# Optimization experiments

Hardware: AMD Instinct MI355X
Metric: run time of the kernel (lower is better)

The kernel has to match this reference:

```python
import jax, jax.numpy as jnp
import numpy as np

B_SZ, N_IN, N_CTX, UNITS, RANK = 4096, 4096, 512, 4096, 256


def setup_inputs() -> dict:
    key = jax.random.key(0)
    ks = jax.random.split(key, 8)
    inputs = jax.random.normal(ks[0], (B_SZ, N_IN), dtype=jnp.float32)
    context = jax.random.normal(ks[1], (B_SZ, N_CTX), dtype=jnp.float32)
    # Orthogonal-ish init approximated by scaled normals (math-equivalent shapes)
    U = jax.random.normal(ks[2], (N_IN, RANK), dtype=jnp.float32) / np.sqrt(N_IN)
    S = jax.random.uniform(ks[3], (RANK,), dtype=jnp.float32, minval=0.5, maxval=1.5)
    V = jax.random.normal(ks[4], (UNITS, RANK), dtype=jnp.float32) / np.sqrt(UNITS)
    W = jax.random.normal(ks[5], (N_CTX, RANK), dtype=jnp.float32) / np.sqrt(N_CTX)
    B = jnp.zeros((RANK,), dtype=jnp.float32)
    bias = jnp.zeros((UNITS,), dtype=jnp.float32)
    return {"inputs": inputs, "context": context, "U": U, "S": S, "V": V, "W": W, "B": B, "bias": bias}


def reference(inputs, context, U, S, V, W, B, bias):
    # chi[b,r] = sigmoid(context @ W + B)
    chi = jax.nn.sigmoid(context @ W + B)                  # [B, R]
    # Original: kernel[b,n,m] = sum_r U[n,r]*S[r]*chi[b,r]*V[m,r];
    # out[b,m] = sum_n x[b,n]*kernel[b,n,m]. Algebraically equal to:
    t = (inputs @ U) * (S * chi)                           # [B, R]
    out = t @ V.T + bias                                   # first '+ self.bias'
    out = out + bias                                       # 'outputs += self.bias' (use_bias=True)
    return jax.nn.relu(out)
```

## Files before the change

kernel.cpp:

```cpp
#include <hip/hip_runtime.h>

#define B_SZ 4096
#define N_IN 4096
#define N_CTX 512
#define UNITS 4096
#define RANK 256
#define ZSPLIT 8

typedef __attribute__((ext_vector_type(8))) __bf16 bf16x8;
typedef __attribute__((ext_vector_type(4))) float f32x4;
typedef __attribute__((ext_vector_type(8))) unsigned short ushort8;

__device__ __forceinline__ unsigned short f2bf(float f) {
    unsigned int u = __float_as_uint(f);
    u += 0x7FFFu + ((u >> 16) & 1u);
    return (unsigned short)(u >> 16);
}
__device__ __forceinline__ unsigned short f2bf_fast(float f) {
    return (unsigned short)((__float_as_uint(f) + 0x8000u) >> 16);
}
__device__ __forceinline__ float bf2f(unsigned short h) {
    return __uint_as_float(((unsigned int)h) << 16);
}
__device__ __forceinline__ bf16x8 ldfrag(const unsigned short* p) {
    ushort8 t = *(const ushort8*)p;
    return __builtin_bit_cast(bf16x8, t);
}
__device__ __forceinline__ bf16x8 cvt8(float4 lo, float4 hi) {
    ushort8 t = { f2bf_fast(lo.x), f2bf_fast(lo.y), f2bf_fast(lo.z), f2bf_fast(lo.w),
                  f2bf_fast(hi.x), f2bf_fast(hi.y), f2bf_fast(hi.z), f2bf_fast(hi.w) };
    return __builtin_bit_cast(bf16x8, t);
}
#define MFMA(a, b, c) __builtin_amdgcn_mfma_f32_16x16x32_bf16((a), (b), (c), 0, 0, 0)

__global__ void prep(const float* __restrict__ U, const float* __restrict__ W,
                     const float* __restrict__ V,
                     unsigned short* __restrict__ UT, unsigned short* __restrict__ WT,
                     unsigned short* __restrict__ Vb) {
    __shared__ unsigned short t[64][66];
    int bid = blockIdx.x, tid = threadIdx.x;
    if (bid < 288) {
        const float* src; unsigned short* dst; int R, C, rb, cb;
        if (bid < 256) { src = U; dst = UT; R = N_IN; C = RANK; rb = (bid & 63) * 64; cb = (bid >> 6) * 64; }
        else { int b = bid - 256; src = W; dst = WT; R = N_CTX; C = RANK; rb = (b & 7) * 64; cb = (b >> 3) * 64; }
        int r = tid >> 4, c4 = (tid & 15) * 4;
        for (int i = 0; i < 4; i++) {
            float4 v = *(const float4*)(src + (size_t)(rb + r + i * 16) * C + cb + c4);
            t[r + i * 16][c4 + 0] = f2bf(v.x);
            t[r + i * 16][c4 + 1] = f2bf(v.y);
            t[r + i * 16][c4 + 2] = f2bf(v.z);
            t[r + i * 16][c4 + 3] = f2bf(v.w);
        }
        __syncthreads();
        int c = tid >> 3, r8 = (tid & 7) * 8;
        for (int j = 0; j < 2; j++) {
            int cc = c + j * 32;
            ushort8 o;
            for (int k = 0; k < 8; k++) o[k] = t[r8 + k][cc];
            *(ushort8*)(dst + (size_t)(cb + cc) * R + rb + r8) = o;
        }
    } else {
        size_t base = (size_t)(bid - 288) * 2048 + (size_t)tid * 8;
        float4 a = *(const float4*)(V + base);
        float4 b = *(const float4*)(V + base + 4);
        ushort8 o = { f2bf(a.x), f2bf(a.y), f2bf(a.z), f2bf(a.w),
                      f2bf(b.x), f2bf(b.y), f2bf(b.z), f2bf(b.w) };
        *(ushort8*)(Vb + base) = o;
    }
}

__launch_bounds__(256, 4)
__global__ void k1_chi(const float* __restrict__ ctx, const unsigned short* __restrict__ WT,
                       const float* __restrict__ S, const float* __restrict__ Bb,
                       unsigned short* __restrict__ Schi) {
    __shared__ unsigned short Bs[64 * 512];
    int tid = threadIdx.x, wv = tid >> 6, lane = tid & 63;
    int ln15 = lane & 15, quad = lane >> 4;
    int n0 = blockIdx.x * 64, mbase = blockIdx.y * 128;
    #pragma unroll
    for (int i = 0; i < 16; i++) {
        int linear = i * 256 + tid;
        int r = linear >> 6, c = linear & 63;
        ushort8 v = *(const ushort8*)(WT + (size_t)(n0 + r) * N_CTX + c * 8);
        *(ushort8*)(Bs + r * 512 + ((c ^ (r & 7)) * 8)) = v;
    }
    __syncthreads();
    int m0 = mbase + wv * 32;
    const float* Xp  = ctx + (size_t)(m0 + ln15) * N_CTX + quad * 8;
    const float* Xp2 = Xp + (size_t)16 * N_CTX;
    f32x4 acc[2][4] = {};
    float4 a[2][2][2];
    a[0][0][0] = *(const float4*)(Xp);  a[0][0][1] = *(const float4*)(Xp + 4);
    a[0][1][0] = *(const float4*)(Xp2); a[0][1][1] = *(const float4*)(Xp2 + 4);
    #pragma unroll
    for (int kt = 0; kt < 16; kt++) {
        int cur = kt & 1, nxt = cur ^ 1;
        if (kt < 15) {
            int ko = (kt + 1) * 32;
            a[nxt][0][0] = *(const float4*)(Xp + ko);  a[nxt][0][1] = *(const float4*)(Xp + ko + 4);
            a[nxt][1][0] = *(const float4*)(Xp2 + ko); a[nxt][1][1] = *(const float4*)(Xp2 + ko + 4);
        }
        bf16x8 bfr[4];
        int sw = ((4 * kt + quad) ^ (ln15 & 7)) * 8;
        #pragma unroll
        for (int j = 0; j < 4; j++) bfr[j] = ldfrag(Bs + (j * 16 + ln15) * 512 + sw);
        bf16x8 af0 = cvt8(a[cur][0][0], a[cur][0][1]);
        bf16x8 af1 = cvt8(a[cur][1][0], a[cur][1][1]);
        #pragma unroll
        for (int j = 0; j < 4; j++) {
            acc[0][j] = MFMA(af0, bfr[j], acc[0][j]);
            acc[1][j] = MFMA(af1, bfr[j], acc[1][j]);
        }
    }
    #pragma unroll
    for (int j = 0; j < 4; j++) {
        int col = n0 + j * 16 + ln15;
        float sv = S[col], bv = Bb[col];
        #pragma unroll
        for (int i = 0; i < 2; i++)
            #pragma unroll
            for (int r = 0; r < 4; r++) {
                int row = m0 + i * 16 + quad * 4 + r;
                float x = acc[i][j][r] + bv;
                Schi[(size_t)row * RANK + col] = f2bf_fast(sv / (1.f + __expf(-x)));
            }
    }
}

__launch_bounds__(512, 4)
__global__ void k2_t0(const float* __restrict__ X, const unsigned short* __restrict__ UT,
                      unsigned short* __restrict__ T0p) {
    __shared__ unsigned short Bs[64 * 512];
    int tid = threadIdx.x, wv = tid >> 6, lane = tid & 63;
    int ln15 = lane & 15, quad = lane >> 4;
    int n0 = blockIdx.x * 64;
    int kbase = blockIdx.y * 512;
    int mbase = blockIdx.z * 256;
    #pragma unroll
    for (int i = 0; i < 8; i++) {
        int linear = i * 512 + tid;
        int r = linear >> 6, c = linear & 63;
        ushort8 v = *(const ushort8*)(UT + (size_t)(n0 + r) * N_IN + kbase + c * 8);
        *(ushort8*)(Bs + r * 512 + ((c ^ (r & 7)) * 8)) = v;
    }
    __syncthreads();
    int m0 = mbase + wv * 32;
    const float* Xp  = X + (size_t)(m0 + ln15) * N_IN + kbase + quad * 8;
    const float* Xp2 = Xp + (size_t)16 * N_IN;
    f32x4 acc[2][4] = {};
    float4 a[2][2][2];
    a[0][0][0] = *(const float4*)(Xp);  a[0][0][1] = *(const float4*)(Xp + 4);
    a[0][1][0] = *(const float4*)(Xp2); a[0][1][1] = *(const float4*)(Xp2 + 4);
    #pragma unroll
    for (int kt = 0; kt < 16; kt++) {
        int cur = kt & 1, nxt = cur ^ 1;
        if (kt < 15) {
            int ko = (kt + 1) * 32;
            a[nxt][0][0] = *(const float4*)(Xp + ko);  a[nxt][0][1] = *(const float4*)(Xp + ko + 4);
            a[nxt][1][0] = *(const float4*)(Xp2 + ko); a[nxt][1][1] = *(const float4*)(Xp2 + ko + 4);
        }
        bf16x8 bfr[4];
        int sw = ((4 * kt + quad) ^ (ln15 & 7)) * 8;
        #pragma unroll
        for (int j = 0; j < 4; j++) bfr[j] = ldfrag(Bs + (j * 16 + ln15) * 512 + sw);
        bf16x8 af0 = cvt8(a[cur][0][0], a[cur][0][1]);
        bf16x8 af1 = cvt8(a[cur][1][0], a[cur][1][1]);
        #pragma unroll
        for (int j = 0; j < 4; j++) {
            acc[0][j] = MFMA(af0, bfr[j], acc[0][j]);
            acc[1][j] = MFMA(af1, bfr[j], acc[1][j]);
        }
    }
    unsigned short* P = T0p + (size_t)blockIdx.y * B_SZ * RANK;
    #pragma unroll
    for (int i = 0; i < 2; i++)
        #pragma unroll
        for (int j = 0; j < 4; j++) {
            int col = n0 + j * 16 + ln15;
            #pragma unroll
            for (int r = 0; r < 4; r++) {
                int row = m0 + i * 16 + quad * 4 + r;
                P[(size_t)row * RANK + col] = f2bf_fast(acc[i][j][r]);
            }
        }
}

__global__ void e_red(const unsigned short* __restrict__ T0p, const unsigned short* __restrict__ Schi,
                      unsigned short* __restrict__ T) {
    int i = blockIdx.x * 256 + threadIdx.x;
    const size_t stride = (size_t)B_SZ * RANK;
    float a[8] = {};
    for (int z = 0; z < ZSPLIT; z++) {
        ushort8 p = *(const ushort8*)(T0p + z * stride + (size_t)i * 8);
        for (int k = 0; k < 8; k++) a[k] += bf2f(p[k]);
    }
    ushort8 s = *(const ushort8*)(Schi + (size_t)i * 8);
    ushort8 o;
    for (int k = 0; k < 8; k++) o[k] = f2bf_fast(a[k] * bf2f(s[k]));
    *(ushort8*)(T + (size_t)i * 8) = o;
}

__launch_bounds__(512, 4)
__global__ void k3_out(const unsigned short* __restrict__ T, const unsigned short* __restrict__ Vb,
                       const float* __restrict__ bias, float* __restrict__ out) {
    __shared__ unsigned short Bs[128 * 256];
    int tid = threadIdx.x, wv = tid >> 6, lane = tid & 63;
    int ln15 = lane & 15, quad = lane >> 4;
    int n0 = blockIdx.x * 128, mbase = blockIdx.y * 128;
    #pragma unroll
    for (int i = 0; i < 8; i++) {
        int linear = i * 512 + tid;
        int r = linear >> 5, c = linear & 31;
        ushort8 v = *(const ushort8*)(Vb + (size_t)(n0 + r) * RANK + c * 8);
        *(ushort8*)(Bs + r * 256 + ((c ^ (r & 7)) * 8)) = v;
    }
    __syncthreads();
    int wm = wv >> 1, wn = wv & 1;
    int m0 = mbase + wm * 32, nb = wn * 64;
    const unsigned short* Ap  = T + (size_t)(m0 + ln15) * RANK + quad * 8;
    const unsigned short* Ap2 = Ap + (size_t)16 * RANK;
    f32x4 acc[2][4] = {};
    ushort8 a[2][2];
    a[0][0] = *(const ushort8*)(Ap);
    a[0][1] = *(const ushort8*)(Ap2);
    #pragma unroll
    for (int kt = 0; kt < 8; kt++) {
        int cur = kt & 1, nxt = cur ^ 1;
        if (kt < 7) {
            int ko = (kt + 1) * 32;
            a[nxt][0] = *(const ushort8*)(Ap + ko);
            a[nxt][1] = *(const ushort8*)(Ap2 + ko);
        }
        bf16x8 bfr[4];
        int sw = ((4 * kt + quad) ^ (ln15 & 7)) * 8;
        #pragma unroll
        for (int j = 0; j < 4; j++) bfr[j] = ldfrag(Bs + (nb + j * 16 + ln15) * 256 + sw);
        bf16x8 af0 = __builtin_bit_cast(bf16x8, a[cur][0]);
        bf16x8 af1 = __builtin_bit_cast(bf16x8, a[cur][1]);
        #pragma unroll
        for (int j = 0; j < 4; j++) {
            acc[0][j] = MFMA(af0, bfr[j], acc[0][j]);
            acc[1][j] = MFMA(af1, bfr[j], acc[1][j]);
        }
    }
    #pragma unroll
    for (int j = 0; j < 4; j++) {
        int col = n0 + nb + j * 16 + ln15;
        float bv = 2.f * bias[col];
        #pragma unroll
        for (int i = 0; i < 2; i++)
            #pragma unroll
            for (int r = 0; r < 4; r++) {
                int row = m0 + i * 16 + quad * 4 + r;
                float v = acc[i][j][r] + bv;
                out[(size_t)row * UNITS + col] = fmaxf(v, 0.f);
            }
    }
}

extern "C" void kernel_launch(void* const* d_in, const int* in_sizes, int n_in,
                              void* d_out, int out_size, void* d_ws, size_t ws_size,
                              hipStream_t stream) {
    (void)in_sizes; (void)n_in; (void)out_size; (void)ws_size;
    const float* inputs  = (const float*)d_in[0];
    const float* context = (const float*)d_in[1];
    const float* U       = (const float*)d_in[2];
    const float* S       = (const float*)d_in[3];
    const float* V       = (const float*)d_in[4];
    const float* W       = (const float*)d_in[5];
    const float* Bb      = (const float*)d_in[6];
    const float* bias    = (const float*)d_in[7];
    float* out = (float*)d_out;

    char* ws = (char*)d_ws;
    size_t o = 0;
    unsigned short* UT   = (unsigned short*)(ws + o); o += (size_t)RANK * N_IN * 2;
    unsigned short* WT   = (unsigned short*)(ws + o); o += (size_t)RANK * N_CTX * 2;
    unsigned short* Vb   = (unsigned short*)(ws + o); o += (size_t)UNITS * RANK * 2;
    unsigned short* Schi = (unsigned short*)(ws + o); o += (size_t)B_SZ * RANK * 2;
    unsigned short* T    = (unsigned short*)(ws + o); o += (size_t)B_SZ * RANK * 2;
    unsigned short* T0p  = (unsigned short*)(ws + o); o += (size_t)ZSPLIT * B_SZ * RANK * 2;

    prep<<<800, 256, 0, stream>>>(U, W, V, UT, WT, Vb);
    k1_chi<<<dim3(4, 32), 256, 0, stream>>>(context, WT, S, Bb, Schi);
    k2_t0<<<dim3(4, 8, 16), 512, 0, stream>>>(inputs, UT, T0p);
    e_red<<<(B_SZ * RANK) / (256 * 8), 256, 0, stream>>>(T0p, Schi, T);
    k3_out<<<dim3(32, 32), 512, 0, stream>>>(T, Vb, bias, out);
}
```

Before: 207.9 us.

## Restructure input GEMM to stage converted X rows in LDS and stream U

The input-projection kernel is reorganized so that each block converts a 16-row slab of X to bf16 once into swizzled shared memory, and warps stream U fragments directly from global with double buffering across a 4-way K split (2 warps per K half). Before, each block staged a U tile in LDS and every block re-read and re-converted fp32 X. The chi and output kernels get smaller tiles (16 rows per warp, 64-column output blocks) for more blocks, and the chi launch now comes after the input GEMM. The trade is less X conversion and re-read traffic against U being read from global or L2 by every block, with no LDS reuse for it.

```diff
diff --git a/kernel.cpp b/kernel.cpp
--- a/kernel.cpp
+++ b/kernel.cpp
@@ -26,10 +26,10 @@
     ushort8 t = *(const ushort8*)p;
     return __builtin_bit_cast(bf16x8, t);
 }
-__device__ __forceinline__ bf16x8 cvt8(float4 lo, float4 hi) {
+__device__ __forceinline__ ushort8 cvt8u(float4 lo, float4 hi) {
     ushort8 t = { f2bf_fast(lo.x), f2bf_fast(lo.y), f2bf_fast(lo.z), f2bf_fast(lo.w),
                   f2bf_fast(hi.x), f2bf_fast(hi.y), f2bf_fast(hi.z), f2bf_fast(hi.w) };
-    return __builtin_bit_cast(bf16x8, t);
+    return t;
 }
 #define MFMA(a, b, c) __builtin_amdgcn_mfma_f32_16x16x32_bf16((a), (b), (c), 0, 0, 0)
 
@@ -76,7 +76,7 @@
     __shared__ unsigned short Bs[64 * 512];
     int tid = threadIdx.x, wv = tid >> 6, lane = tid & 63;
     int ln15 = lane & 15, quad = lane >> 4;
-    int n0 = blockIdx.x * 64, mbase = blockIdx.y * 128;
+    int n0 = blockIdx.x * 64, mbase = blockIdx.y * 64;
     #pragma unroll
     for (int i = 0; i < 16; i++) {
         int linear = i * 256 + tid;
@@ -85,104 +85,97 @@
         *(ushort8*)(Bs + r * 512 + ((c ^ (r & 7)) * 8)) = v;
     }
     __syncthreads();
-    int m0 = mbase + wv * 32;
-    const float* Xp  = ctx + (size_t)(m0 + ln15) * N_CTX + quad * 8;
-    const float* Xp2 = Xp + (size_t)16 * N_CTX;
-    f32x4 acc[2][4] = {};
-    float4 a[2][2][2];
-    a[0][0][0] = *(const float4*)(Xp);  a[0][0][1] = *(const float4*)(Xp + 4);
-    a[0][1][0] = *(const float4*)(Xp2); a[0][1][1] = *(const float4*)(Xp2 + 4);
+    int m0 = mbase + wv * 16;
+    const float* Xp = ctx + (size_t)(m0 + ln15) * N_CTX + quad * 8;
+    f32x4 acc[4] = {};
+    float4 a[2][2];
+    a[0][0] = *(const float4*)(Xp); a[0][1] = *(const float4*)(Xp + 4);
     #pragma unroll
     for (int kt = 0; kt < 16; kt++) {
         int cur = kt & 1, nxt = cur ^ 1;
         if (kt < 15) {
             int ko = (kt + 1) * 32;
-            a[nxt][0][0] = *(const float4*)(Xp + ko);  a[nxt][0][1] = *(const float4*)(Xp + ko + 4);
-            a[nxt][1][0] = *(const float4*)(Xp2 + ko); a[nxt][1][1] = *(const float4*)(Xp2 + ko + 4);
+            a[nxt][0] = *(const float4*)(Xp + ko); a[nxt][1] = *(const float4*)(Xp + ko + 4);
         }
         bf16x8 bfr[4];
-        int sw = ((4 * kt + quad) ^ (ln15 & 7)) * 8;
-        #pragma unroll
-        for (int j = 0; j < 4; j++) bfr[j] = ldfrag(Bs + (j * 16 + ln15) * 512 + sw);
-        bf16x8 af0 = cvt8(a[cur][0][0], a[cur][0][1]);
-        bf16x8 af1 = cvt8(a[cur][1][0], a[cur][1][1]);
-        #pragma unroll
-        for (int j = 0; j < 4; j++) {
-            acc[0][j] = MFMA(af0, bfr[j], acc[0][j]);
-            acc[1][j] = MFMA(af1, bfr[j], acc[1][j]);
-        }
+        int sw8 = ((4 * kt + quad) ^ (ln15 & 7)) * 8;
+        #pragma unroll
+        for (int j = 0; j < 4; j++) bfr[j] = ldfrag(Bs + (j * 16 + ln15) * 512 + sw8);
+        bf16x8 af = __builtin_bit_cast(bf16x8, cvt8u(a[cur][0], a[cur][1]));
+        #pragma unroll
+        for (int j = 0; j < 4; j++) acc[j] = MFMA(af, bfr[j], acc[j]);
     }
     #pragma unroll
     for (int j = 0; j < 4; j++) {
         int col = n0 + j * 16 + ln15;
         float sv = S[col], bv = Bb[col];
         #pragma unroll
-        for (int i = 0; i < 2; i++)
-            #pragma unroll
-            for (int r = 0; r < 4; r++) {
-                int row = m0 + i * 16 + quad * 4 + r;
-                float x = acc[i][j][r] + bv;
-                Schi[(size_t)row * RANK + col] = f2bf_fast(sv / (1.f + __expf(-x)));
-            }
-    }
-}
-
-__launch_bounds__(512, 4)
+        for (int r = 0; r < 4; r++) {
+            int row = m0 + quad * 4 + r;
+            float x = acc[j][r] + bv;
+            Schi[(size_t)row * RANK + col] = f2bf_fast(sv / (1.f + __expf(-x)));
+        }
+    }
+}
+
+__launch_bounds__(256, 4)
 __global__ void k2_t0(const float* __restrict__ X, const unsigned short* __restrict__ UT,
                       unsigned short* __restrict__ T0p) {
-    __shared__ unsigned short Bs[64 * 512];
+    __shared__ unsigned short Xs[16 * 1024];
     int tid = threadIdx.x, wv = tid >> 6, lane = tid & 63;
     int ln15 = lane & 15, quad = lane >> 4;
-    int n0 = blockIdx.x * 64;
-    int kbase = blockIdx.y * 512;
-    int mbase = blockIdx.z * 256;
-    #pragma unroll
-    for (int i = 0; i < 8; i++) {
-        int linear = i * 512 + tid;
-        int r = linear >> 6, c = linear & 63;
-        ushort8 v = *(const ushort8*)(UT + (size_t)(n0 + r) * N_IN + kbase + c * 8);
-        *(ushort8*)(Bs + r * 512 + ((c ^ (r & 7)) * 8)) = v;
+    int mbase = blockIdx.x * 16;
+    int kbase = blockIdx.y * 1024;
+    {
+        int r = tid >> 4, tc = tid & 15;
+        const float* src = X + (size_t)(mbase + r) * N_IN + kbase;
+        unsigned short* drow = Xs + r * 1024;
+        #pragma unroll
+        for (int s = 0; s < 8; s++) {
+            int j = tc + s * 16;
+            float4 lo = *(const float4*)(src + j * 8);
+            float4 hi = *(const float4*)(src + j * 8 + 4);
+            *(ushort8*)(drow + ((j ^ (r & 7)) * 8)) = cvt8u(lo, hi);
+        }
     }
     __syncthreads();
-    int m0 = mbase + wv * 32;
-    const float* Xp  = X + (size_t)(m0 + ln15) * N_IN + kbase + quad * 8;
-    const float* Xp2 = Xp + (size_t)16 * N_IN;
-    f32x4 acc[2][4] = {};
-    float4 a[2][2][2];
-    a[0][0][0] = *(const float4*)(Xp);  a[0][0][1] = *(const float4*)(Xp + 4);
-    a[0][1][0] = *(const float4*)(Xp2); a[0][1][1] = *(const float4*)(Xp2 + 4);
+    int ni = wv & 1, ki = wv >> 1;
+    int n0 = ni * 128;
+    const unsigned short* Bp = UT + (size_t)(n0 + ln15) * N_IN + kbase + ki * 512 + quad * 8;
+    const unsigned short* Arow = Xs + ln15 * 1024;
+    int abase = ki * 64;
+    f32x4 acc[8] = {};
+    ushort8 b[2][8];
+    #pragma unroll
+    for (int j = 0; j < 8; j++) b[0][j] = *(const ushort8*)(Bp + (size_t)j * 16 * N_IN);
+    bf16x8 afc = ldfrag(Arow + (((abase + quad) ^ (ln15 & 7)) * 8));
     #pragma unroll
     for (int kt = 0; kt < 16; kt++) {
         int cur = kt & 1, nxt = cur ^ 1;
+        bf16x8 afn = afc;
         if (kt < 15) {
-            int ko = (kt + 1) * 32;
-            a[nxt][0][0] = *(const float4*)(Xp + ko);  a[nxt][0][1] = *(const float4*)(Xp + ko + 4);
-            a[nxt][1][0] = *(const float4*)(Xp2 + ko); a[nxt][1][1] = *(const float4*)(Xp2 + ko + 4);
-        }
-        bf16x8 bfr[4];
-        int sw = ((4 * kt + quad) ^ (ln15 & 7)) * 8;
-        #pragma unroll
-        for (int j = 0; j < 4; j++) bfr[j] = ldfrag(Bs + (j * 16 + ln15) * 512 + sw);
-        bf16x8 af0 = cvt8(a[cur][0][0], a[cur][0][1]);
-        bf16x8 af1 = cvt8(a[cur][1][0], a[cur][1][1]);
-        #pragma unroll
-        for (int j = 0; j < 4; j++) {
-            acc[0][j] = MFMA(af0, bfr[j], acc[0][j]);
-            acc[1][j] = MFMA(af1, bfr[j], acc[1][j]);
-        }
-    }
-    unsigned short* P = T0p + (size_t)blockIdx.y * B_SZ * RANK;
-    #pragma unroll
-    for (int i = 0; i < 2; i++)
-        #pragma unroll
-        for (int j = 0; j < 4; j++) {
-            int col = n0 + j * 16 + ln15;
+            const unsigned short* Bp2 = Bp + (kt + 1) * 32;
             #pragma unroll
-            for (int r = 0; r < 4; r++) {
-                int row = m0 + i * 16 + quad * 4 + r;
-                P[(size_t)row * RANK + col] = f2bf_fast(acc[i][j][r]);
-            }
-        }
+            for (int j = 0; j < 8; j++) b[nxt][j] = *(const ushort8*)(Bp2 + (size_t)j * 16 * N_IN);
+            int ch = abase + (kt + 1) * 4 + quad;
+            afn = ldfrag(Arow + ((ch ^ (ln15 & 7)) * 8));
+        }
+        #pragma unroll
+        for (int j = 0; j < 8; j++)
+            acc[j] = MFMA(afc, __builtin_bit_cast(bf16x8, b[cur][j]), acc[j]);
+        afc = afn;
+    }
+    int z = blockIdx.y * 2 + ki;
+    unsigned short* P = T0p + (size_t)z * B_SZ * RANK;
+    #pragma unroll
+    for (int j = 0; j < 8; j++) {
+        int col = n0 + j * 16 + ln15;
+        #pragma unroll
+        for (int r = 0; r < 4; r++) {
+            int row = mbase + quad * 4 + r;
+            P[(size_t)row * RANK + col] = f2bf_fast(acc[j][r]);
+        }
+    }
 }
 
 __global__ void e_red(const unsigned short* __restrict__ T0p, const unsigned short* __restrict__ Schi,
@@ -200,23 +193,22 @@
     *(ushort8*)(T + (size_t)i * 8) = o;
 }
 
-__launch_bounds__(512, 4)
+__launch_bounds__(256, 4)
 __global__ void k3_out(const unsigned short* __restrict__ T, const unsigned short* __restrict__ Vb,
                        const float* __restrict__ bias, float* __restrict__ out) {
-    __shared__ unsigned short Bs[128 * 256];
+    __shared__ unsigned short Bs[64 * 256];
     int tid = threadIdx.x, wv = tid >> 6, lane = tid & 63;
     int ln15 = lane & 15, quad = lane >> 4;
-    int n0 = blockIdx.x * 128, mbase = blockIdx.y * 128;
+    int n0 = blockIdx.x * 64, mbase = blockIdx.y * 128;
     #pragma unroll
     for (int i = 0; i < 8; i++) {
-        int linear = i * 512 + tid;
+        int linear = i * 256 + tid;
         int r = linear >> 5, c = linear & 31;
         ushort8 v = *(const ushort8*)(Vb + (size_t)(n0 + r) * RANK + c * 8);
         *(ushort8*)(Bs + r * 256 + ((c ^ (r & 7)) * 8)) = v;
     }
     __syncthreads();
-    int wm = wv >> 1, wn = wv & 1;
-    int m0 = mbase + wm * 32, nb = wn * 64;
+    int m0 = mbase + wv * 32;
     const unsigned short* Ap  = T + (size_t)(m0 + ln15) * RANK + quad * 8;
     const unsigned short* Ap2 = Ap + (size_t)16 * RANK;
     f32x4 acc[2][4] = {};
@@ -232,9 +224,9 @@
             a[nxt][1] = *(const ushort8*)(Ap2 + ko);
         }
         bf16x8 bfr[4];
-        int sw = ((4 * kt + quad) ^ (ln15 & 7)) * 8;
-        #pragma unroll
-        for (int j = 0; j < 4; j++) bfr[j] = ldfrag(Bs + (nb + j * 16 + ln15) * 256 + sw);
+        int sw8 = ((4 * kt + quad) ^ (ln15 & 7)) * 8;
+        #pragma unroll
+        for (int j = 0; j < 4; j++) bfr[j] = ldfrag(Bs + (j * 16 + ln15) * 256 + sw8);
         bf16x8 af0 = __builtin_bit_cast(bf16x8, a[cur][0]);
         bf16x8 af1 = __builtin_bit_cast(bf16x8, a[cur][1]);
         #pragma unroll
@@ -245,7 +237,7 @@
     }
     #pragma unroll
     for (int j = 0; j < 4; j++) {
-        int col = n0 + nb + j * 16 + ln15;
+        int col = n0 + j * 16 + ln15;
         float bv = 2.f * bias[col];
         #pragma unroll
         for (int i = 0; i < 2; i++)
@@ -282,8 +274,8 @@
     unsigned short* T0p  = (unsigned short*)(ws + o); o += (size_t)ZSPLIT * B_SZ * RANK * 2;
 
     prep<<<800, 256, 0, stream>>>(U, W, V, UT, WT, Vb);
-    k1_chi<<<dim3(4, 32), 256, 0, stream>>>(context, WT, S, Bb, Schi);
-    k2_t0<<<dim3(4, 8, 16), 512, 0, stream>>>(inputs, UT, T0p);
+    k2_t0<<<dim3(256, 4), 256, 0, stream>>>(inputs, UT, T0p);
+    k1_chi<<<dim3(4, 64), 256, 0, stream>>>(context, WT, S, Bb, Schi);
     e_red<<<(B_SZ * RANK) / (256 * 8), 256, 0, stream>>>(T0p, Schi, T);
-    k3_out<<<dim3(32, 32), 512, 0, stream>>>(T, Vb, bias, out);
-}
+    k3_out<<<dim3(64, 32), 256, 0, stream>>>(T, Vb, bias, out);
+}
```

Measured after the change: 225.5 us. 8.5% more time.
